# Kernel optimization log

Measured on AMD Instinct MI355X. Metric: run time of the kernel, lower is better.

The kernel has to match this reference:

```python
import jax, jax.numpy as jnp
import numpy as np

BS, N, NDIMS, HNF, HID = 32, 512, 3, 6, 64
NORM_CONSTANT = 1.0
EPS = 1e-8


def remove_mean_with_mask(x, node_mask):
    n = jnp.sum(node_mask, axis=1, keepdims=True)  # [bs,1,1]
    mean = jnp.sum(x, axis=1, keepdims=True) / n
    return x - mean * node_mask


def setup_inputs() -> dict:
    key = jax.random.key(0)
    k0, k1, k2 = jax.random.split(key, 3)
    xh = jax.random.normal(k0, (BS, N, NDIMS + HNF), dtype=jnp.float32)
    node_mask = jnp.ones((BS, N, 1), dtype=jnp.float32)
    # feature_embedding: Linear(6,64) -> SiLU -> Linear(64,2)
    W1 = jax.random.normal(k1, (HNF, HID), dtype=jnp.float32) * 0.1
    b1 = jnp.zeros((HID,), dtype=jnp.float32)
    W2 = jax.random.normal(k2, (HID, 2), dtype=jnp.float32) * 0.1
    b2 = jnp.zeros((2,), dtype=jnp.float32)
    return {"xh": xh, "node_mask": node_mask, "W1": W1, "b1": b1, "W2": W2, "b2": b2}


def reference(xh, node_mask, W1, b1, W2, b2):
    # x_input = remove_mean_with_mask(xh[..., :3], node_mask)
    x = remove_mean_with_mask(xh[..., :NDIMS], node_mask)  # [bs,n,3]
    # coord2diff over the dense fully-connected edge set (row=i, col=j):
    # coord_diff[b,i,j] = x[b,i] - x[b,j]
    coord_diff = x[:, :, None, :] - x[:, None, :, :]        # [bs,n,n,3]
    radial = jnp.sum(coord_diff ** 2, axis=-1, keepdims=True)  # [bs,n,n,1]
    norm = jnp.sqrt(radial + EPS)
    coord_diff = coord_diff / (norm + NORM_CONSTANT)
    # feature_embedding MLP on node features h = xh[..., 3:]
    h = xh[..., NDIMS:]                                      # [bs,n,6]
    h_emb = jax.nn.silu(h @ W1 + b1) @ W2 + b2               # [bs,n,2]
    # node-pair gather: h_i = h_emb[rows], h_j = h_emb[cols]
    h_i = jnp.broadcast_to(h_emb[:, :, None, :], (BS, N, N, 2))
    h_j = jnp.broadcast_to(h_emb[:, None, :, :], (BS, N, N, 2))
    # edge_features = cat([radial, coord_diff, h_i, h_j], -1) -> [bs,n,n,8]
    edge_features = jnp.concatenate([radial, coord_diff, h_i, h_j], axis=-1)
    return edge_features
```

## Files before the change

### kernel.cpp

```cpp
#include <hip/hip_runtime.h>
#include <math.h>

#define BS 32
#define NN 512
#define NDIMS 3
#define HNF 6
#define HID 64
#define EPSV 1e-8f
#define NORMC 1.0f
#define ROWS 8

__global__ __launch_bounds__(512) void prep_kernel(
    const float* __restrict__ xh,
    const float* __restrict__ mask,
    const float* __restrict__ W1,
    const float* __restrict__ b1,
    const float* __restrict__ W2,
    const float* __restrict__ b2,
    float* __restrict__ xc,
    float* __restrict__ hemb)
{
    const int b = blockIdx.x;
    const int i = threadIdx.x;

    __shared__ float s_red[8][4];
    __shared__ float s_mean[3];
    __shared__ float sW1[HNF * HID];
    __shared__ float sb1[HID];
    __shared__ float sW2[HID * 2];
    __shared__ float sb2[2];

    for (int t = i; t < HNF * HID; t += 512) sW1[t] = W1[t];
    if (i < HID) sb1[i] = b1[i];
    for (int t = i; t < HID * 2; t += 512) sW2[t] = W2[t];
    if (i < 2)   sb2[i] = b2[i];

    const float* row = xh + ((size_t)b * NN + i) * (NDIMS + HNF);
    float x0 = row[0], x1 = row[1], x2 = row[2];
    float h[HNF];
    #pragma unroll
    for (int k = 0; k < HNF; ++k) h[k] = row[NDIMS + k];
    float m = mask[(size_t)b * NN + i];

    float v0 = x0, v1 = x1, v2 = x2, vm = m;
    #pragma unroll
    for (int off = 32; off > 0; off >>= 1) {
        v0 += __shfl_down(v0, off);
        v1 += __shfl_down(v1, off);
        v2 += __shfl_down(v2, off);
        vm += __shfl_down(vm, off);
    }
    const int lane = i & 63, wave = i >> 6;
    if (lane == 0) {
        s_red[wave][0] = v0; s_red[wave][1] = v1;
        s_red[wave][2] = v2; s_red[wave][3] = vm;
    }
    __syncthreads();
    if (i == 0) {
        float t0 = 0.f, t1 = 0.f, t2 = 0.f, tm = 0.f;
        #pragma unroll
        for (int w = 0; w < 8; ++w) {
            t0 += s_red[w][0]; t1 += s_red[w][1];
            t2 += s_red[w][2]; tm += s_red[w][3];
        }
        s_mean[0] = t0 / tm; s_mean[1] = t1 / tm; s_mean[2] = t2 / tm;
    }
    __syncthreads();

    float cx0 = x0 - s_mean[0] * m;
    float cx1 = x1 - s_mean[1] * m;
    float cx2 = x2 - s_mean[2] * m;
    float* xo = xc + ((size_t)b * NN + i) * 3;
    xo[0] = cx0; xo[1] = cx1; xo[2] = cx2;

    float acc0 = sb2[0], acc1 = sb2[1];
    #pragma unroll 8
    for (int hh = 0; hh < HID; ++hh) {
        float z = sb1[hh];
        #pragma unroll
        for (int k = 0; k < HNF; ++k) z += h[k] * sW1[k * HID + hh];
        float s = z / (1.0f + expf(-z));
        acc0 += s * sW2[hh * 2 + 0];
        acc1 += s * sW2[hh * 2 + 1];
    }
    float* ho = hemb + ((size_t)b * NN + i) * 2;
    ho[0] = acc0; ho[1] = acc1;
}

__global__ __launch_bounds__(512) void edge_kernel(
    const float* __restrict__ xc,
    const float* __restrict__ hemb,
    float4* __restrict__ out4)
{
    const int blk = blockIdx.x;
    const int bi0 = blk * ROWS;
    const int b   = bi0 >> 9;
    const int i0  = bi0 & (NN - 1);
    const int j   = threadIdx.x;

    __shared__ float sx[NN * 3];
    __shared__ float sh[NN * 2];

    const float* xb = xc   + (size_t)b * NN * 3;
    const float* hb = hemb + (size_t)b * NN * 2;
    sx[j]        = xb[j];
    sx[j + 512]  = xb[j + 512];
    sx[j + 1024] = xb[j + 1024];
    sh[j]        = hb[j];
    sh[j + 512]  = hb[j + 512];
    __syncthreads();

    const int ja = j >> 1;
    const int jb = 256 + ja;
    const bool odd = (j & 1) != 0;

    const float xa0 = sx[ja * 3 + 0], xa1 = sx[ja * 3 + 1], xa2 = sx[ja * 3 + 2];
    const float xb0 = sx[jb * 3 + 0], xb1 = sx[jb * 3 + 1], xb2 = sx[jb * 3 + 2];
    const float ha0 = sh[ja * 2 + 0], ha1 = sh[ja * 2 + 1];
    const float hb0 = sh[jb * 2 + 0], hb1 = sh[jb * 2 + 1];

    float4* rowout = out4 + (size_t)bi0 * NN * 2;

    #pragma unroll
    for (int r = 0; r < ROWS; ++r) {
        const int i = i0 + r;
        const float xi0 = sx[i * 3 + 0], xi1 = sx[i * 3 + 1], xi2 = sx[i * 3 + 2];
        const float hi0 = sh[i * 2 + 0], hi1 = sh[i * 2 + 1];

        float d0 = xi0 - xa0, d1 = xi1 - xa1, d2 = xi2 - xa2;
        float rada = d0 * d0 + d1 * d1 + d2 * d2;
        float inva = __builtin_amdgcn_rcpf(__builtin_amdgcn_sqrtf(rada + EPSV) + NORMC);
        float4 va = odd ? make_float4(hi0, hi1, ha0, ha1)
                        : make_float4(rada, d0 * inva, d1 * inva, d2 * inva);

        float e0 = xi0 - xb0, e1 = xi1 - xb1, e2 = xi2 - xb2;
        float radb = e0 * e0 + e1 * e1 + e2 * e2;
        float invb = __builtin_amdgcn_rcpf(__builtin_amdgcn_sqrtf(radb + EPSV) + NORMC);
        float4 vb = odd ? make_float4(hi0, hi1, hb0, hb1)
                        : make_float4(radb, e0 * invb, e1 * invb, e2 * invb);

        rowout[j]       = va;
        rowout[j + 512] = vb;
        rowout += NN * 2;
    }
}

extern "C" void kernel_launch(void* const* d_in, const int* in_sizes, int n_in,
                              void* d_out, int out_size, void* d_ws, size_t ws_size,
                              hipStream_t stream) {
    const float* xh   = (const float*)d_in[0];
    const float* mask = (const float*)d_in[1];
    const float* W1   = (const float*)d_in[2];
    const float* b1   = (const float*)d_in[3];
    const float* W2   = (const float*)d_in[4];
    const float* b2   = (const float*)d_in[5];

    float* xc   = (float*)d_ws;
    float* hemb = xc + (size_t)BS * NN * 3;

    prep_kernel<<<BS, 512, 0, stream>>>(xh, mask, W1, b1, W2, b2, xc, hemb);
    edge_kernel<<<BS * NN / ROWS, 512, 0, stream>>>(xc, hemb, (float4*)d_out);
}
```

Measured before the change: 276.8 us.

## Fuse prep into edge kernel, recomputing node data per block with nontemporal stores

Merges the per-batch centering and feature MLP kernel into the edge kernel. Each block now reloads its batch's full xh slice into LDS and recomputes the mean and the MLP embedding for all 512 nodes, which removes one kernel launch and the workspace round trip. Rows per block go from 8 to 16 to spread that recompute over more output, and output writes use nontemporal stores. The cost is 32x redundant MLP work per batch and much larger LDS use per block, which may lower occupancy.

```diff
diff --git a/kernel.cpp b/kernel.cpp
--- a/kernel.cpp
+++ b/kernel.cpp
@@ -8,39 +8,47 @@
 #define HID 64
 #define EPSV 1e-8f
 #define NORMC 1.0f
-#define ROWS 8
+#define ROWS 16
 
-__global__ __launch_bounds__(512) void prep_kernel(
+typedef float f32x4 __attribute__((ext_vector_type(4)));
+
+__global__ __launch_bounds__(512) void fused_edge_kernel(
     const float* __restrict__ xh,
     const float* __restrict__ mask,
     const float* __restrict__ W1,
     const float* __restrict__ b1,
     const float* __restrict__ W2,
     const float* __restrict__ b2,
-    float* __restrict__ xc,
-    float* __restrict__ hemb)
+    f32x4* __restrict__ out4)
 {
-    const int b = blockIdx.x;
-    const int i = threadIdx.x;
+    const int blk = blockIdx.x;
+    const int b   = blk >> 5;
+    const int i0  = (blk & 31) * ROWS;
+    const int j   = threadIdx.x;
 
-    __shared__ float s_red[8][4];
-    __shared__ float s_mean[3];
+    __shared__ float sxh[NN * 9];
+    __shared__ float sx[NN * 3];
+    __shared__ float sh[NN * 2];
     __shared__ float sW1[HNF * HID];
     __shared__ float sb1[HID];
     __shared__ float sW2[HID * 2];
-    __shared__ float sb2[2];
+    __shared__ float s_red[8][4];
+    __shared__ float s_mean[3];
 
-    for (int t = i; t < HNF * HID; t += 512) sW1[t] = W1[t];
-    if (i < HID) sb1[i] = b1[i];
-    for (int t = i; t < HID * 2; t += 512) sW2[t] = W2[t];
-    if (i < 2)   sb2[i] = b2[i];
+    const float* xb = xh + (size_t)b * NN * 9;
+    #pragma unroll
+    for (int t = 0; t < 9; ++t) sxh[j + t * 512] = xb[j + t * 512];
+    if (j < HNF * HID) sW1[j] = W1[j];
+    else if (j < HNF * HID + HID) sb1[j - HNF * HID] = b1[j - HNF * HID];
+    if (j < HID * 2) sW2[j] = W2[j];
+    const float sb2_0 = b2[0], sb2_1 = b2[1];
+    const float m = mask[(size_t)b * NN + j];
+    __syncthreads();
 
-    const float* row = xh + ((size_t)b * NN + i) * (NDIMS + HNF);
-    float x0 = row[0], x1 = row[1], x2 = row[2];
+    const float x0 = sxh[j * 9 + 0], x1 = sxh[j * 9 + 1], x2 = sxh[j * 9 + 2];
     float h[HNF];
     #pragma unroll
-    for (int k = 0; k < HNF; ++k) h[k] = row[NDIMS + k];
-    float m = mask[(size_t)b * NN + i];
+    for (int k = 0; k < HNF; ++k) h[k] = sxh[j * 9 + 3 + k];
 
     float v0 = x0, v1 = x1, v2 = x2, vm = m;
     #pragma unroll
@@ -50,13 +58,13 @@
         v2 += __shfl_down(v2, off);
         vm += __shfl_down(vm, off);
     }
-    const int lane = i & 63, wave = i >> 6;
+    const int lane = j & 63, wave = j >> 6;
     if (lane == 0) {
         s_red[wave][0] = v0; s_red[wave][1] = v1;
         s_red[wave][2] = v2; s_red[wave][3] = vm;
     }
     __syncthreads();
-    if (i == 0) {
+    if (j == 0) {
         float t0 = 0.f, t1 = 0.f, t2 = 0.f, tm = 0.f;
         #pragma unroll
         for (int w = 0; w < 8; ++w) {
@@ -67,13 +75,11 @@
     }
     __syncthreads();
 
-    float cx0 = x0 - s_mean[0] * m;
-    float cx1 = x1 - s_mean[1] * m;
-    float cx2 = x2 - s_mean[2] * m;
-    float* xo = xc + ((size_t)b * NN + i) * 3;
-    xo[0] = cx0; xo[1] = cx1; xo[2] = cx2;
+    sx[j * 3 + 0] = x0 - s_mean[0] * m;
+    sx[j * 3 + 1] = x1 - s_mean[1] * m;
+    sx[j * 3 + 2] = x2 - s_mean[2] * m;
 
-    float acc0 = sb2[0], acc1 = sb2[1];
+    float acc0 = sb2_0, acc1 = sb2_1;
     #pragma unroll 8
     for (int hh = 0; hh < HID; ++hh) {
         float z = sb1[hh];
@@ -83,31 +89,8 @@
         acc0 += s * sW2[hh * 2 + 0];
         acc1 += s * sW2[hh * 2 + 1];
     }
-    float* ho = hemb + ((size_t)b * NN + i) * 2;
-    ho[0] = acc0; ho[1] = acc1;
-}
-
-__global__ __launch_bounds__(512) void edge_kernel(
-    const float* __restrict__ xc,
-    const float* __restrict__ hemb,
-    float4* __restrict__ out4)
-{
-    const int blk = blockIdx.x;
-    const int bi0 = blk * ROWS;
-    const int b   = bi0 >> 9;
-    const int i0  = bi0 & (NN - 1);
-    const int j   = threadIdx.x;
-
-    __shared__ float sx[NN * 3];
-    __shared__ float sh[NN * 2];
-
-    const float* xb = xc   + (size_t)b * NN * 3;
-    const float* hb = hemb + (size_t)b * NN * 2;
-    sx[j]        = xb[j];
-    sx[j + 512]  = xb[j + 512];
-    sx[j + 1024] = xb[j + 1024];
-    sh[j]        = hb[j];
-    sh[j + 512]  = hb[j + 512];
+    sh[j * 2 + 0] = acc0;
+    sh[j * 2 + 1] = acc1;
     __syncthreads();
 
     const int ja = j >> 1;
@@ -119,9 +102,9 @@
     const float ha0 = sh[ja * 2 + 0], ha1 = sh[ja * 2 + 1];
     const float hb0 = sh[jb * 2 + 0], hb1 = sh[jb * 2 + 1];
 
-    float4* rowout = out4 + (size_t)bi0 * NN * 2;
+    f32x4* rowout = out4 + ((size_t)b * NN + i0) * NN * 2;
 
-    #pragma unroll
+    #pragma unroll 4
     for (int r = 0; r < ROWS; ++r) {
         const int i = i0 + r;
         const float xi0 = sx[i * 3 + 0], xi1 = sx[i * 3 + 1], xi2 = sx[i * 3 + 2];
@@ -130,17 +113,19 @@
         float d0 = xi0 - xa0, d1 = xi1 - xa1, d2 = xi2 - xa2;
         float rada = d0 * d0 + d1 * d1 + d2 * d2;
         float inva = __builtin_amdgcn_rcpf(__builtin_amdgcn_sqrtf(rada + EPSV) + NORMC);
-        float4 va = odd ? make_float4(hi0, hi1, ha0, ha1)
-                        : make_float4(rada, d0 * inva, d1 * inva, d2 * inva);
+        f32x4 va;
+        if (odd) { va.x = hi0; va.y = hi1; va.z = ha0; va.w = ha1; }
+        else     { va.x = rada; va.y = d0 * inva; va.z = d1 * inva; va.w = d2 * inva; }
 
         float e0 = xi0 - xb0, e1 = xi1 - xb1, e2 = xi2 - xb2;
         float radb = e0 * e0 + e1 * e1 + e2 * e2;
         float invb = __builtin_amdgcn_rcpf(__builtin_amdgcn_sqrtf(radb + EPSV) + NORMC);
-        float4 vb = odd ? make_float4(hi0, hi1, hb0, hb1)
-                        : make_float4(radb, e0 * invb, e1 * invb, e2 * invb);
+        f32x4 vb;
+        if (odd) { vb.x = hi0; vb.y = hi1; vb.z = hb0; vb.w = hb1; }
+        else     { vb.x = radb; vb.y = e0 * invb; vb.z = e1 * invb; vb.w = e2 * invb; }
 
-        rowout[j]       = va;
-        rowout[j + 512] = vb;
+        __builtin_nontemporal_store(va, &rowout[j]);
+        __builtin_nontemporal_store(vb, &rowout[j + 512]);
         rowout += NN * 2;
     }
 }
@@ -155,9 +140,6 @@
     const float* W2   = (const float*)d_in[4];
     const float* b2   = (const float*)d_in[5];
 
-    float* xc   = (float*)d_ws;
-    float* hemb = xc + (size_t)BS * NN * 3;
-
-    prep_kernel<<<BS, 512, 0, stream>>>(xh, mask, W1, b1, W2, b2, xc, hemb);
-    edge_kernel<<<BS * NN / ROWS, 512, 0, stream>>>(xc, hemb, (float4*)d_out);
+    fused_edge_kernel<<<BS * (NN / ROWS), 512, 0, stream>>>(
+        xh, mask, W1, b1, W2, b2, (f32x4*)d_out);
 }
```

Result: slower. 285.5 us (+3.2%).
